# Kernel tuning notes

Measured on AMD Instinct MI355X. Metric: run time of the kernel, lower is better.

The kernel has to match this reference:

```python
import jax, jax.numpy as jnp
import numpy as np

HEADS = 8
DIM_HEAD = 64
EPS = 1e-4


def softmax_kernel(data, proj, is_query):
    # data: [b,h,n,d], proj: [m,d]
    data_normalizer = data.shape[-1] ** -0.25
    ratio = proj.shape[0] ** -0.5
    data_dash = jnp.einsum('bhnd,md->bhnm', data_normalizer * data, proj)
    diag = (data * data).sum(-1) * 0.5 * (data_normalizer ** 2)  # [b,h,n]
    diag = diag[..., None]
    if is_query:
        stab = jnp.max(data_dash, axis=-1, keepdims=True)
    else:
        stab = jnp.max(data_dash)
    return ratio * (jnp.exp(data_dash - diag - stab) + EPS)


def linear_attention(q, k, v):
    # q,k: [b,h,n,m], v: [b,h,n,e]
    k_cumsum = k.sum(axis=-2)  # [b,h,m]
    d_inv = 1.0 / jnp.einsum('bhnm,bhm->bhn', q, k_cumsum)
    context = jnp.einsum('bhnm,bhne->bhme', k, v)  # [b,h,m,e]
    return jnp.einsum('bhme,bhnm,bhn->bhne', context, q, d_inv)


def setup_inputs() -> dict:
    key = jax.random.key(0)
    ks = jax.random.split(key, 6)
    b, n, dim = 8, 4096, 512
    m, dh = 266, DIM_HEAD
    x = jax.random.normal(ks[0], (b, n, dim), dtype=jnp.float32)
    s = dim ** -0.5
    Wq = jax.random.normal(ks[1], (dim, dim), dtype=jnp.float32) * s
    Wk = jax.random.normal(ks[2], (dim, dim), dtype=jnp.float32) * s
    Wv = jax.random.normal(ks[3], (dim, dim), dtype=jnp.float32) * s
    Wo = jax.random.normal(ks[4], (dim, dim), dtype=jnp.float32) * s
    bo = jnp.zeros((dim,), dtype=jnp.float32)
    proj = jax.random.normal(ks[5], (m, dh), dtype=jnp.float32)
    return {"x": x, "Wq": Wq, "Wk": Wk, "Wv": Wv, "Wo": Wo, "bo": bo, "proj": proj}


def reference(x, Wq, Wk, Wv, Wv_unused=None, *, _=None, **__):
    raise NotImplementedError


def reference(x, Wq, Wk, Wv, Wo, bo, proj):
    b, n, dim = x.shape
    h, dh = HEADS, DIM_HEAD
    # Linear projections (weights stored as [in, out])
    q = (x @ Wq).reshape(b, n, h, dh).transpose(0, 2, 1, 3)  # [b,h,n,dh]
    k = (x @ Wk).reshape(b, n, h, dh).transpose(0, 2, 1, 3)
    v = (x @ Wv).reshape(b, n, h, dh).transpose(0, 2, 1, 3)
    qp = softmax_kernel(q, proj, is_query=True)   # [b,h,n,m]
    kp = softmax_kernel(k, proj, is_query=False)  # [b,h,n,m]
    out = linear_attention(qp, kp, v)             # [b,h,n,dh]
    out = out.transpose(0, 2, 1, 3).reshape(b, n, h * dh)
    return out @ Wo + bo
```

## Files before the change

### kernel.cpp

```cpp
#include <hip/hip_runtime.h>
#include <stdint.h>

#define B_ 8
#define N_ 4096
#define H_ 8
#define DH_ 64
#define DIM_ 512
#define M_ 266
#define MP_ 320
#define BH_ 64
#define BNROWS_ 32768
#define NS_ 8
#define CN_ 0.35355339059327373f
#define RATIO_ 0.06131393394849658f
#define EPS_ 1e-4f
#define REPS_ (RATIO_ * EPS_)

typedef __bf16 bf16x8 __attribute__((ext_vector_type(8)));
typedef float f32x4 __attribute__((ext_vector_type(4)));

union U8 { bf16x8 v; uint4 u; uint2 u2[2]; uint16_t s[8]; };

__device__ __forceinline__ uint32_t f2bf(float f) {
  uint32_t u = __float_as_uint(f);
  u += 0x7FFFu + ((u >> 16) & 1u);
  return u >> 16;
}
__device__ __forceinline__ uint32_t pkbf(float a, float b) {
  uint32_t r;
  asm("v_cvt_pk_bf16_f32 %0, %1, %2" : "=v"(r) : "v"(a), "v"(b));
  return r;
}
__device__ __forceinline__ float bflo(uint32_t u) { return __uint_as_float(u << 16); }
__device__ __forceinline__ float bfhi(uint32_t u) { return __uint_as_float(u & 0xFFFF0000u); }
__device__ __forceinline__ void unp8(uint4 u, float* f) {
  f[0] = bflo(u.x); f[1] = bfhi(u.x); f[2] = bflo(u.y); f[3] = bfhi(u.y);
  f[4] = bflo(u.z); f[5] = bfhi(u.z); f[6] = bflo(u.w); f[7] = bfhi(u.w);
}
__device__ __forceinline__ float f4get(const float4& v, int i) {
  return ((const float*)&v)[i];
}
__device__ __forceinline__ uint32_t fenc(float f) {
  uint32_t u = __float_as_uint(f);
  return u ^ ((uint32_t)((int32_t)u >> 31) | 0x80000000u);
}
__device__ __forceinline__ float fdec(uint32_t e) {
  uint32_t u = (e & 0x80000000u) ? (e ^ 0x80000000u) : ~e;
  return __uint_as_float(u);
}
__device__ __forceinline__ int piperm(int p) {
  int tmt = p >> 4, r = p & 15;
  return 32 * (tmt >> 1) + 8 * (r >> 2) + 4 * (tmt & 1) + (r & 3);
}
__device__ __forceinline__ int phinv(int r) {
  int lo = r & 15;
  return 8 * (lo >> 2) + (lo & 3) + ((r >> 4) << 2);
}
__device__ __forceinline__ void glds16(const uint16_t* g, uint16_t* l) {
  __builtin_amdgcn_global_load_lds(
      (const __attribute__((address_space(1))) void*)g,
      (__attribute__((address_space(3))) void*)l, 16, 0, 0);
}

__global__ void init_stab(uint32_t* s) { *s = fenc(-3.4e38f); }

__global__ __launch_bounds__(256) void cast_x(const float* __restrict__ x,
                                              uint16_t* __restrict__ xb, int n4) {
  int i = blockIdx.x * 256 + threadIdx.x;
  if (i >= n4) return;
  float4 v = ((const float4*)x)[i];
  uint2 o;
  o.x = f2bf(v.x) | (f2bf(v.y) << 16);
  o.y = f2bf(v.z) | (f2bf(v.w) << 16);
  ((uint2*)xb)[i] = o;
}

__global__ __launch_bounds__(256) void cast_wt(const float* __restrict__ w,
                                               uint16_t* __restrict__ wt) {
  int i = blockIdx.x * 256 + threadIdx.x;
  int k = i >> 9, n = i & 511;
  wt[(size_t)n * 512 + k] = (uint16_t)f2bf(w[i]);
}

__global__ __launch_bounds__(256) void cast_projb(const float* __restrict__ proj,
                                                  uint16_t* __restrict__ projb) {
  int i = blockIdx.x * 256 + threadIdx.x;
  if (i >= MP_ * DH_) return;
  int p = i >> 6, d = i & 63;
  int pi = piperm(p);
  float v = (pi < M_) ? proj[pi * DH_ + d] : 0.f;
  projb[i] = (uint16_t)f2bf(v);
}

template <int EPI>
__global__ __launch_bounds__(256) void gemm_glds(const uint16_t* __restrict__ A,
                                                 const uint16_t* __restrict__ Bt,
                                                 float* __restrict__ outF,
                                                 const float* __restrict__ bias,
                                                 uint16_t* __restrict__ qb,
                                                 uint16_t* __restrict__ kbuf,
                                                 uint16_t* __restrict__ vTb) {
  __shared__ __align__(16) uint16_t As[2][128 * 32];
  __shared__ __align__(16) uint16_t Bs[2][128 * 32];
  const int t = threadIdx.x, lane = t & 63, w = t >> 6;
  const int g = lane >> 4, r16 = lane & 15;
  const int wr = (w >> 1) * 64, wc = (w & 1) * 64;
  const int flat = blockIdx.x;
  const int xcd = flat & 7, jj = flat >> 3;
  const int bx = xcd * 32 + (jj & 31);
  const int by = jj >> 5;
  const size_t rowA0 = (size_t)bx * 128;
  const size_t rowB0 = (size_t)by * 128;
  const int K = 512;

  f32x4 acc[4][4];
#pragma unroll
  for (int i = 0; i < 4; ++i)
#pragma unroll
    for (int j = 0; j < 4; ++j) acc[i][j] = (f32x4){0.f, 0.f, 0.f, 0.f};

  auto stageG = [&](int kt, int buf) {
#pragma unroll
    for (int s = 0; s < 2; ++s) {
      const int row = w * 32 + s * 16;
      const uint16_t* ga = A + (rowA0 + row + (lane >> 2)) * (size_t)K + kt * 32 + (lane & 3) * 8;
      glds16(ga, &As[buf][row * 32]);
      const uint16_t* gb = Bt + (rowB0 + row + (lane >> 2)) * (size_t)K + kt * 32 + (lane & 3) * 8;
      glds16(gb, &Bs[buf][row * 32]);
    }
  };
  stageG(0, 0);
  for (int kt = 0; kt < 16; ++kt) {
    __syncthreads();
    if (kt + 1 < 16) stageG(kt + 1, (kt + 1) & 1);
    const uint16_t* as = As[kt & 1];
    const uint16_t* bs = Bs[kt & 1];
    bf16x8 af[4], bfr[4];
#pragma unroll
    for (int i = 0; i < 4; ++i)
      af[i] = *(const bf16x8*)&as[(wr + i * 16 + r16) * 32 + g * 8];
#pragma unroll
    for (int j = 0; j < 4; ++j)
      bfr[j] = *(const bf16x8*)&bs[(wc + j * 16 + r16) * 32 + g * 8];
#pragma unroll
    for (int i = 0; i < 4; ++i)
#pragma unroll
      for (int j = 0; j < 4; ++j)
        acc[i][j] = __builtin_amdgcn_mfma_f32_16x16x32_bf16(af[i], bfr[j], acc[i][j], 0, 0, 0);
  }
  const int region = by >> 2;
  const int lcolBase = (by & 3) * 128;
#pragma unroll
  for (int i = 0; i < 4; ++i) {
    const size_t row0 = rowA0 + wr + i * 16 + g * 4;
#pragma unroll
    for (int j = 0; j < 4; ++j) {
      if constexpr (EPI == 0) {
        const size_t col = rowB0 + wc + j * 16 + r16;
        float badd = bias ? bias[col] : 0.f;
#pragma unroll
        for (int q = 0; q < 4; ++q)
          outF[(row0 + q) * (size_t)512 + col] = acc[i][j][q] + badd;
      } else {
        const int lcol = lcolBase + wc + j * 16 + r16;
        if (region == 2) {
          int bb = (int)(row0 >> 12), n = (int)(row0 & 4095);
          int hh = lcol >> 6, e = lcol & 63;
          uint2 o;
          o.x = pkbf(acc[i][j][0], acc[i][j][1]);
          o.y = pkbf(acc[i][j][2], acc[i][j][3]);
          *(uint2*)&vTb[((size_t)((bb * 8 + hh) * 64 + e)) * 4096 + n] = o;
        } else {
          uint16_t* dst = region ? kbuf : qb;
#pragma unroll
          for (int q = 0; q < 4; ++q)
            dst[(row0 + q) * (size_t)512 + lcol] = (uint16_t)f2bf(acc[i][j][q]);
        }
      }
    }
  }
}

__global__ __launch_bounds__(256) void stab2_mfma(const uint16_t* __restrict__ kb,
                                                  const uint16_t* __restrict__ projb,
                                                  uint32_t* __restrict__ stab) {
  __shared__ uint16_t kt[2][32][72];
  __shared__ float wred[4];
  const int t = threadIdx.x, lane = t & 63, w = t >> 6;
  const int g = lane >> 4, r16 = lane & 15;
  const int bh = blockIdx.x, ns = blockIdx.y;
  const int b = bh >> 3, h = bh & 7;
  bf16x8 pj[5][2];
  bool mval[5];
#pragma unroll
  for (int mt = 0; mt < 5; ++mt) {
    int m16 = mt * 64 + w * 16;
    pj[mt][0] = *(const bf16x8*)&projb[(m16 + r16) * 64 + g * 8];
    pj[mt][1] = *(const bf16x8*)&projb[(m16 + r16) * 64 + 32 + g * 8];
    mval[mt] = piperm(m16 + r16) < M_;
  }
  auto stage = [&](int it, int buf) {
    int n0 = ns * 128 + it * 32;
    int row = t >> 3, c8 = t & 7;
    *(uint4*)&kt[buf][row][c8 * 8] =
        *(const uint4*)&kb[((size_t)(b * N_ + n0 + row)) * DIM_ + h * DH_ + c8 * 8];
  };
  stage(0, 0);
  __syncthreads();
  float vmax = -3.4e38f;
  for (int it = 0; it < 4; ++it) {
    int cur = it & 1;
    if (it + 1 < 4) stage(it + 1, cur ^ 1);
    bf16x8 ka[2][2];
#pragma unroll
    for (int nsub = 0; nsub < 2; ++nsub) {
      ka[nsub][0] = *(const bf16x8*)&kt[cur][nsub * 16 + r16][g * 8];
      ka[nsub][1] = *(const bf16x8*)&kt[cur][nsub * 16 + r16][32 + g * 8];
    }
#pragma unroll
    for (int mt = 0; mt < 5; ++mt) {
#pragma unroll
      for (int nsub = 0; nsub < 2; ++nsub) {
        f32x4 c4 = (f32x4){0.f, 0.f, 0.f, 0.f};
        c4 = __builtin_amdgcn_mfma_f32_16x16x32_bf16(ka[nsub][0], pj[mt][0], c4, 0, 0, 0);
        c4 = __builtin_amdgcn_mfma_f32_16x16x32_bf16(ka[nsub][1], pj[mt][1], c4, 0, 0, 0);
        if (mval[mt])
          vmax = fmaxf(vmax, fmaxf(fmaxf(c4[0], c4[1]), fmaxf(c4[2], c4[3])));
      }
    }
    __syncthreads();
  }
#pragma unroll
  for (int off = 32; off; off >>= 1) vmax = fmaxf(vmax, __shfl_xor(vmax, off));
  if (lane == 0) wred[w] = vmax;
  __syncthreads();
  if (t == 0) {
    float m = fmaxf(fmaxf(wred[0], wred[1]), fmaxf(wred[2], wred[3]));
    atomicMax(stab, fenc(CN_ * m));
  }
}

__global__ __launch_bounds__(256) void ctx_mfma(const uint16_t* __restrict__ kb,
                                                const uint16_t* __restrict__ vTb,
                                                const uint16_t* __restrict__ projb,
                                                const uint32_t* __restrict__ stab_e,
                                                uint16_t* __restrict__ ctxpb,
                                                float* __restrict__ kcump) {
  __shared__ uint16_t kt[2][32][72];
  __shared__ uint16_t vt[2][64][40];
  __shared__ float dk2[2][32];
  __shared__ uint16_t kpb[4][16][40];
  const int t = threadIdx.x, lane = t & 63, w = t >> 6;
  const int g = lane >> 4, r16 = lane & 15;
  const int mt = blockIdx.x, bh = blockIdx.y, ns = blockIdx.z;
  const int b = bh >> 3, h = bh & 7;
  const int m16 = mt * 64 + w * 16;
  const float stab = fdec(*stab_e);
  const bool mvalid = piperm(m16 + r16) < M_;
  bf16x8 pj0 = *(const bf16x8*)&projb[(m16 + r16) * 64 + g * 8];
  bf16x8 pj1 = *(const bf16x8*)&projb[(m16 + r16) * 64 + 32 + g * 8];
  const int iters = 4096 / (32 * NS_);

  auto stage = [&](int it, int buf) {
    int n0 = (ns * iters + it) * 32;
    {
      int row = t >> 3, c8 = t & 7;
      uint4 kv = *(const uint4*)&kb[((size_t)(b * N_ + n0 + row)) * DIM_ + h * DH_ + c8 * 8];
      *(uint4*)&kt[buf][row][c8 * 8] = kv;
      float f[8]; unp8(kv, f);
      float sq = f[0]*f[0]+f[1]*f[1]+f[2]*f[2]+f[3]*f[3]+f[4]*f[4]+f[5]*f[5]+f[6]*f[6]+f[7]*f[7];
      sq += __shfl_xor(sq, 1); sq += __shfl_xor(sq, 2); sq += __shfl_xor(sq, 4);
      if (c8 == 0) dk2[buf][row] = 0.5f * CN_ * CN_ * sq;
    }
    {
      int e = t >> 2, c = t & 3;
      uint4 vv = *(const uint4*)&vTb[((size_t)(bh * 64 + e)) * 4096 + n0 + c * 8];
      *(uint4*)&vt[buf][e][c * 8] = vv;
    }
  };
  f32x4 acc[4];
#pragma unroll
  for (int j = 0; j < 4; ++j) acc[j] = (f32x4){0.f, 0.f, 0.f, 0.f};
  float kcacc = 0.f;

  stage(0, 0);
  __syncthreads();
  for (int it = 0; it < iters; ++it) {
    int cur = it & 1;
    if (it + 1 < iters) stage(it + 1, cur ^ 1);
#pragma unroll
    for (int nsub = 0; nsub < 2; ++nsub) {
      bf16x8 ka0 = *(const bf16x8*)&kt[cur][nsub * 16 + r16][g * 8];
      bf16x8 ka1 = *(const bf16x8*)&kt[cur][nsub * 16 + r16][32 + g * 8];
      f32x4 c4 = (f32x4){0.f, 0.f, 0.f, 0.f};
      c4 = __builtin_amdgcn_mfma_f32_16x16x32_bf16(ka0, pj0, c4, 0, 0, 0);
      c4 = __builtin_amdgcn_mfma_f32_16x16x32_bf16(ka1, pj1, c4, 0, 0, 0);
      float4 dkv = *(const float4*)&dk2[cur][nsub * 16 + 4 * g];
      float kp[4];
#pragma unroll
      for (int q = 0; q < 4; ++q) {
        float arg = CN_ * c4[q] - f4get(dkv, q) - stab;
        float e = RATIO_ * __expf(arg) + REPS_;
        kp[q] = mvalid ? e : 0.f;
        kcacc += kp[q];
      }
      *(uint2*)&kpb[w][r16][nsub * 16 + 4 * g] = make_uint2(pkbf(kp[0], kp[1]), pkbf(kp[2], kp[3]));
    }
    U8 kq; kq.u = *(const uint4*)&kpb[w][r16][g * 8];
#pragma unroll
    for (int j = 0; j < 4; ++j) {
      U8 vf; vf.u = *(const uint4*)&vt[cur][j * 16 + r16][g * 8];
      acc[j] = __builtin_amdgcn_mfma_f32_16x16x32_bf16(kq.v, vf.v, acc[j], 0, 0, 0);
    }
    __syncthreads();
  }
#pragma unroll
  for (int j = 0; j < 4; ++j) {
    uint2 o;
    o.x = pkbf(acc[j][0], acc[j][1]);
    o.y = pkbf(acc[j][2], acc[j][3]);
    *(uint2*)&ctxpb[(((size_t)ns * BH_ + bh) * 64 + j * 16 + r16) * MP_ + m16 + 4 * g] = o;
  }
  kcacc += __shfl_xor(kcacc, 16);
  kcacc += __shfl_xor(kcacc, 32);
  if (lane < 16) kcump[((size_t)ns * BH_ + bh) * MP_ + m16 + lane] = kcacc;
}

__global__ __launch_bounds__(256) void merge_kernel(const uint16_t* __restrict__ ctxpb,
                                                    const float* __restrict__ kcump,
                                                    uint16_t* __restrict__ ctxgb,
                                                    float* __restrict__ kcumg) {
  int idx = blockIdx.x * 256 + threadIdx.x;
  const int total = BH_ * 64 * MP_;
  if (idx < total) {
    float s = 0.f;
#pragma unroll
    for (int p = 0; p < NS_; ++p)
      s += __uint_as_float((uint32_t)ctxpb[(size_t)p * total + idx] << 16);
    int row = idx / MP_;
    int pos = idx - row * MP_;
    int col = (pos & ~31) + phinv(pos & 31);
    ctxgb[(size_t)row * MP_ + col] = (uint16_t)f2bf(s);
  }
  const int ktotal = BH_ * MP_;
  if (idx < ktotal) {
    float s = 0.f;
#pragma unroll
    for (int p = 0; p < NS_; ++p) s += kcump[(size_t)p * ktotal + idx];
    kcumg[idx] = s;
  }
}

__global__ __launch_bounds__(512) void attn_mfma(const uint16_t* __restrict__ qb,
                                                 const uint16_t* __restrict__ projb,
                                                 const uint16_t* __restrict__ ctxgb,
                                                 const float* __restrict__ kcumg,
                                                 uint16_t* __restrict__ attnb) {
  __shared__ uint16_t ctile[64][328];
  __shared__ uint16_t qs[128][72];
  __shared__ float kcums[MP_];
  __shared__ float dqs[128];
  __shared__ float denb[8][16];
  const int t = threadIdx.x, lane = t & 63, w = t >> 6;
  const int g = lane >> 4, r16 = lane & 15;
  const int nch = blockIdx.x, bh = blockIdx.y;
  const int b = bh >> 3, h = bh & 7;
  {
    int row = t >> 3, cb = t & 7;
#pragma unroll
    for (int cc = 0; cc < 5; ++cc) {
      int cN = cb * 40 + cc * 8;
      *(uint4*)&ctile[row][cN] = *(const uint4*)&ctxgb[((size_t)bh * 64 + row) * MP_ + cN];
    }
  }
  if (t < MP_) kcums[t] = kcumg[(size_t)bh * MP_ + t];

  for (int it = 0; it < 4; ++it) {
    const int nbase = nch * 512 + it * 128;
    __syncthreads();
    {
      int row = t >> 2, c2 = t & 3;
      float sq = 0.f;
#pragma unroll
      for (int cc = 0; cc < 2; ++cc) {
        int c8 = c2 * 2 + cc;
        uint4 qv = *(const uint4*)&qb[((size_t)(b * N_ + nbase + row)) * DIM_ + h * DH_ + c8 * 8];
        *(uint4*)&qs[row][c8 * 8] = qv;
        float f[8]; unp8(qv, f);
        sq += f[0]*f[0]+f[1]*f[1]+f[2]*f[2]+f[3]*f[3]+f[4]*f[4]+f[5]*f[5]+f[6]*f[6]+f[7]*f[7];
      }
      sq += __shfl_xor(sq, 1); sq += __shfl_xor(sq, 2);
      if (c2 == 0) dqs[row] = 0.5f * CN_ * CN_ * sq;
    }
    __syncthreads();
    bf16x8 qf0 = *(const bf16x8*)&qs[w * 16 + r16][g * 8];
    bf16x8 qf1 = *(const bf16x8*)&qs[w * 16 + r16][32 + g * 8];
    f32x4 S[18];
#pragma unroll
    for (int mt = 0; mt < 18; ++mt) {
      bf16x8 pa0 = *(const bf16x8*)&projb[(mt * 16 + r16) * 64 + g * 8];
      bf16x8 pa1 = *(const bf16x8*)&projb[(mt * 16 + r16) * 64 + 32 + g * 8];
      f32x4 c4 = (f32x4){0.f, 0.f, 0.f, 0.f};
      c4 = __builtin_amdgcn_mfma_f32_16x16x32_bf16(pa0, qf0, c4, 0, 0, 0);
      S[mt] = __builtin_amdgcn_mfma_f32_16x16x32_bf16(pa1, qf1, c4, 0, 0, 0);
    }
    float rmax = -3.4e38f;
#pragma unroll
    for (int mt = 0; mt < 18; ++mt) {
#pragma unroll
      for (int q = 0; q < 4; ++q) {
        bool val = (mt < 16) || (256 + 4 * (mt & 1) + 8 * g + q < M_);
        if (val) rmax = fmaxf(rmax, CN_ * S[mt][q]);
      }
    }
    rmax = fmaxf(rmax, __shfl_xor(rmax, 16));
    rmax = fmaxf(rmax, __shfl_xor(rmax, 32));
    const float offv = rmax + dqs[w * 16 + r16];
    float denp = 0.f;
    uint32_t pk[18][2];
#pragma unroll
    for (int mt = 0; mt < 18; ++mt) {
      float4 kc4 = *(const float4*)&kcums[mt * 16 + 4 * g];
      float qp[4];
#pragma unroll
      for (int q = 0; q < 4; ++q) {
        bool val = (mt < 16) || (256 + 4 * (mt & 1) + 8 * g + q < M_);
        float e = RATIO_ * __expf(CN_ * S[mt][q] - offv) + REPS_;
        qp[q] = val ? e : 0.f;
        denp += qp[q] * f4get(kc4, q);
      }
      pk[mt][0] = pkbf(qp[0], qp[1]);
      pk[mt][1] = pkbf(qp[2], qp[3]);
    }
    denp += __shfl_xor(denp, 16);
    denp += __shfl_xor(denp, 32);
    if (lane < 16) denb[w][lane] = denp;
    f32x4 o[4];
#pragma unroll
    for (int j = 0; j < 4; ++j) o[j] = (f32x4){0.f, 0.f, 0.f, 0.f};
#pragma unroll
    for (int s = 0; s < 9; ++s) {
      U8 af; af.u = make_uint4(pk[2 * s][0], pk[2 * s][1], pk[2 * s + 1][0], pk[2 * s + 1][1]);
#pragma unroll
      for (int j = 0; j < 4; ++j) {
        U8 cf; cf.u = *(const uint4*)&ctile[j * 16 + r16][s * 32 + g * 8];
        o[j] = __builtin_amdgcn_mfma_f32_16x16x32_bf16(af.v, cf.v, o[j], 0, 0, 0);
      }
    }
    float4 dv = *(const float4*)&denb[w][4 * g];
    float rd[4];
#pragma unroll
    for (int q = 0; q < 4; ++q) rd[q] = 1.0f / f4get(dv, q);
#pragma unroll
    for (int j = 0; j < 4; ++j) {
#pragma unroll
      for (int q = 0; q < 4; ++q) {
        float val = o[j][q] * rd[q];
        int n = nbase + w * 16 + 4 * g + q;
        attnb[((size_t)(b * N_ + n)) * DIM_ + h * DH_ + j * 16 + r16] = (uint16_t)f2bf(val);
      }
    }
  }
}

extern "C" void kernel_launch(void* const* d_in, const int* in_sizes, int n_in,
                              void* d_out, int out_size, void* d_ws, size_t ws_size,
                              hipStream_t stream) {
  const float* x = (const float*)d_in[0];
  const float* Wq = (const float*)d_in[1];
  const float* Wk = (const float*)d_in[2];
  const float* Wv = (const float*)d_in[3];
  const float* Wo = (const float*)d_in[4];
  const float* bo = (const float*)d_in[5];
  const float* proj = (const float*)d_in[6];
  float* out = (float*)d_out;

  char* ws = (char*)d_ws;
  size_t off = 0;
  auto alloc = [&](size_t bytes) {
    char* p = ws + off;
    off += (bytes + 255) & ~(size_t)255;
    return p;
  };
  uint16_t* wqkvT = (uint16_t*)alloc((size_t)1536 * 512 * 2);
  uint16_t* woT = (uint16_t*)alloc((size_t)512 * 512 * 2);
  uint16_t* projb = (uint16_t*)alloc((size_t)MP_ * DH_ * 2);
  uint16_t* vTb = (uint16_t*)alloc((size_t)BNROWS_ * DIM_ * 2);
  uint16_t* ctxpb = (uint16_t*)alloc((size_t)NS_ * BH_ * 64 * MP_ * 2);
  float* kcump = (float*)alloc((size_t)NS_ * BH_ * MP_ * 4);
  uint16_t* ctxgb = (uint16_t*)alloc((size_t)BH_ * 64 * MP_ * 2);
  float* kcumg = (float*)alloc((size_t)BH_ * MP_ * 4);
  uint32_t* stab = (uint32_t*)alloc(256);
  uint16_t* xb = (uint16_t*)alloc((size_t)BNROWS_ * DIM_ * 2);
  uint16_t* qb = (uint16_t*)d_out;
  uint16_t* kb = qb + (size_t)BNROWS_ * DIM_;
  uint16_t* attnb = vTb;

  init_stab<<<1, 1, 0, stream>>>(stab);
  cast_wt<<<1024, 256, 0, stream>>>(Wq, wqkvT);
  cast_wt<<<1024, 256, 0, stream>>>(Wk, wqkvT + (size_t)512 * 512);
  cast_wt<<<1024, 256, 0, stream>>>(Wv, wqkvT + (size_t)1024 * 512);
  cast_wt<<<1024, 256, 0, stream>>>(Wo, woT);
  cast_projb<<<80, 256, 0, stream>>>(proj, projb);
  cast_x<<<16384, 256, 0, stream>>>(x, xb, BNROWS_ * DIM_ / 4);

  gemm_glds<1><<<3072, 256, 0, stream>>>(xb, wqkvT, nullptr, nullptr, qb, kb, vTb);

  stab2_mfma<<<dim3(64, 32), 256, 0, stream>>>(kb, projb, stab);
  ctx_mfma<<<dim3(5, 64, NS_), 256, 0, stream>>>(kb, vTb, projb, stab, ctxpb, kcump);
  merge_kernel<<<5120, 256, 0, stream>>>(ctxpb, kcump, ctxgb, kcumg);
  attn_mfma<<<dim3(8, 64), 512, 0, stream>>>(qb, projb, ctxgb, kcumg, attnb);
  gemm_glds<0><<<1024, 256, 0, stream>>>(attnb, woT, out, bo, nullptr, nullptr, nullptr);
}
```

Baseline: 313.1 us.

## Stage GEMM and attention epilogues through LDS for coalesced 16-byte stores

```diff
diff --git a/kernel.cpp b/kernel.cpp
--- a/kernel.cpp
+++ b/kernel.cpp
@@ -92,7 +92,7 @@
   projb[i] = (uint16_t)f2bf(v);
 }
 
-template <int EPI>
+template <int EPI, int NBY>
 __global__ __launch_bounds__(256) void gemm_glds(const uint16_t* __restrict__ A,
                                                  const uint16_t* __restrict__ Bt,
                                                  float* __restrict__ outF,
@@ -100,15 +100,17 @@
                                                  uint16_t* __restrict__ qb,
                                                  uint16_t* __restrict__ kbuf,
                                                  uint16_t* __restrict__ vTb) {
-  __shared__ __align__(16) uint16_t As[2][128 * 32];
-  __shared__ __align__(16) uint16_t Bs[2][128 * 32];
+  __shared__ __align__(16) uint16_t smem[17408];
+  uint16_t (*AsArr)[4096] = (uint16_t (*)[4096])smem;
+  uint16_t (*BsArr)[4096] = (uint16_t (*)[4096])(smem + 8192);
+  uint16_t (*epi)[136] = (uint16_t (*)[136])smem;
   const int t = threadIdx.x, lane = t & 63, w = t >> 6;
   const int g = lane >> 4, r16 = lane & 15;
   const int wr = (w >> 1) * 64, wc = (w & 1) * 64;
   const int flat = blockIdx.x;
   const int xcd = flat & 7, jj = flat >> 3;
-  const int bx = xcd * 32 + (jj & 31);
-  const int by = jj >> 5;
+  const int bxoff = jj / NBY, by = jj - bxoff * NBY;
+  const int bx = xcd * 32 + bxoff;
   const size_t rowA0 = (size_t)bx * 128;
   const size_t rowB0 = (size_t)by * 128;
   const int K = 512;
@@ -124,17 +126,17 @@
     for (int s = 0; s < 2; ++s) {
       const int row = w * 32 + s * 16;
       const uint16_t* ga = A + (rowA0 + row + (lane >> 2)) * (size_t)K + kt * 32 + (lane & 3) * 8;
-      glds16(ga, &As[buf][row * 32]);
+      glds16(ga, &AsArr[buf][row * 32]);
       const uint16_t* gb = Bt + (rowB0 + row + (lane >> 2)) * (size_t)K + kt * 32 + (lane & 3) * 8;
-      glds16(gb, &Bs[buf][row * 32]);
+      glds16(gb, &BsArr[buf][row * 32]);
     }
   };
   stageG(0, 0);
   for (int kt = 0; kt < 16; ++kt) {
     __syncthreads();
     if (kt + 1 < 16) stageG(kt + 1, (kt + 1) & 1);
-    const uint16_t* as = As[kt & 1];
-    const uint16_t* bs = Bs[kt & 1];
+    const uint16_t* as = AsArr[kt & 1];
+    const uint16_t* bs = BsArr[kt & 1];
     bf16x8 af[4], bfr[4];
 #pragma unroll
     for (int i = 0; i < 4; ++i)
@@ -148,34 +150,59 @@
       for (int j = 0; j < 4; ++j)
         acc[i][j] = __builtin_amdgcn_mfma_f32_16x16x32_bf16(af[i], bfr[j], acc[i][j], 0, 0, 0);
   }
-  const int region = by >> 2;
-  const int lcolBase = (by & 3) * 128;
-#pragma unroll
-  for (int i = 0; i < 4; ++i) {
-    const size_t row0 = rowA0 + wr + i * 16 + g * 4;
-#pragma unroll
-    for (int j = 0; j < 4; ++j) {
-      if constexpr (EPI == 0) {
+  if constexpr (EPI == 0) {
+#pragma unroll
+    for (int i = 0; i < 4; ++i) {
+      const size_t row0 = rowA0 + wr + i * 16 + g * 4;
+#pragma unroll
+      for (int j = 0; j < 4; ++j) {
         const size_t col = rowB0 + wc + j * 16 + r16;
         float badd = bias ? bias[col] : 0.f;
 #pragma unroll
         for (int q = 0; q < 4; ++q)
           outF[(row0 + q) * (size_t)512 + col] = acc[i][j][q] + badd;
-      } else {
-        const int lcol = lcolBase + wc + j * 16 + r16;
-        if (region == 2) {
-          int bb = (int)(row0 >> 12), n = (int)(row0 & 4095);
-          int hh = lcol >> 6, e = lcol & 63;
-          uint2 o;
-          o.x = pkbf(acc[i][j][0], acc[i][j][1]);
-          o.y = pkbf(acc[i][j][2], acc[i][j][3]);
-          *(uint2*)&vTb[((size_t)((bb * 8 + hh) * 64 + e)) * 4096 + n] = o;
-        } else {
-          uint16_t* dst = region ? kbuf : qb;
+      }
+    }
+  } else {
+    const int region = by >> 2;
+    const int lcolBase = (by & 3) * 128;
+    __syncthreads();
+    if (region <= 1) {
+#pragma unroll
+      for (int i = 0; i < 4; ++i)
+#pragma unroll
+        for (int j = 0; j < 4; ++j)
 #pragma unroll
           for (int q = 0; q < 4; ++q)
-            dst[(row0 + q) * (size_t)512 + lcol] = (uint16_t)f2bf(acc[i][j][q]);
-        }
+            epi[wr + i * 16 + g * 4 + q][wc + j * 16 + r16] = (uint16_t)f2bf(acc[i][j][q]);
+    } else {
+#pragma unroll
+      for (int i = 0; i < 4; ++i)
+#pragma unroll
+        for (int j = 0; j < 4; ++j)
+#pragma unroll
+          for (int q = 0; q < 4; ++q)
+            epi[wc + j * 16 + r16][wr + i * 16 + g * 4 + q] = (uint16_t)f2bf(acc[i][j][q]);
+    }
+    __syncthreads();
+    const int srow = t >> 4, scol = (t & 15) * 8;
+    if (region <= 1) {
+      uint16_t* dst = region ? kbuf : qb;
+#pragma unroll
+      for (int pass = 0; pass < 8; ++pass) {
+        const int row = pass * 16 + srow;
+        uint4 v = *(const uint4*)&epi[row][scol];
+        *(uint4*)&dst[(rowA0 + row) * (size_t)512 + lcolBase + scol] = v;
+      }
+    } else {
+      const int bb = (int)(rowA0 >> 12), nmod = (int)(rowA0 & 4095);
+#pragma unroll
+      for (int pass = 0; pass < 8; ++pass) {
+        const int erow = pass * 16 + srow;
+        const int lcol = lcolBase + erow;
+        const int hh = lcol >> 6, e = lcol & 63;
+        uint4 v = *(const uint4*)&epi[erow][scol];
+        *(uint4*)&vTb[((size_t)((bb * 8 + hh) * 64 + e)) * 4096 + nmod + scol] = v;
       }
     }
   }
@@ -451,13 +478,20 @@
     float rd[4];
 #pragma unroll
     for (int q = 0; q < 4; ++q) rd[q] = 1.0f / f4get(dv, q);
-#pragma unroll
-    for (int j = 0; j < 4; ++j) {
-#pragma unroll
-      for (int q = 0; q < 4; ++q) {
-        float val = o[j][q] * rd[q];
-        int n = nbase + w * 16 + 4 * g + q;
-        attnb[((size_t)(b * N_ + n)) * DIM_ + h * DH_ + j * 16 + r16] = (uint16_t)f2bf(val);
+    __syncthreads();
+#pragma unroll
+    for (int j = 0; j < 4; ++j)
+#pragma unroll
+      for (int q = 0; q < 4; ++q)
+        qs[w * 16 + 4 * g + q][j * 16 + r16] = (uint16_t)f2bf(o[j][q] * rd[q]);
+    __syncthreads();
+    {
+      const int srow = t >> 3, scol = (t & 7) * 8;
+#pragma unroll
+      for (int pass = 0; pass < 2; ++pass) {
+        const int row = pass * 64 + srow;
+        uint4 v = *(const uint4*)&qs[row][scol];
+        *(uint4*)&attnb[((size_t)(b * N_ + nbase + row)) * DIM_ + h * DH_ + scol] = v;
       }
     }
   }
@@ -504,11 +538,11 @@
   cast_projb<<<80, 256, 0, stream>>>(proj, projb);
   cast_x<<<16384, 256, 0, stream>>>(x, xb, BNROWS_ * DIM_ / 4);
 
-  gemm_glds<1><<<3072, 256, 0, stream>>>(xb, wqkvT, nullptr, nullptr, qb, kb, vTb);
+  gemm_glds<1, 12><<<3072, 256, 0, stream>>>(xb, wqkvT, nullptr, nullptr, qb, kb, vTb);
 
   stab2_mfma<<<dim3(64, 32), 256, 0, stream>>>(kb, projb, stab);
   ctx_mfma<<<dim3(5, 64, NS_), 256, 0, stream>>>(kb, vTb, projb, stab, ctxpb, kcump);
   merge_kernel<<<5120, 256, 0, stream>>>(ctxpb, kcump, ctxgb, kcumg);
   attn_mfma<<<dim3(8, 64), 512, 0, stream>>>(qb, projb, ctxgb, kcumg, attnb);
-  gemm_glds<0><<<1024, 256, 0, stream>>>(attnb, woT, out, bo, nullptr, nullptr, nullptr);
-}
+  gemm_glds<0, 4><<<1024, 256, 0, stream>>>(attnb, woT, out, bo, nullptr, nullptr, nullptr);
+}
```

Result: faster. 295.9 us (-5.5%).
